# Kernel tuning notes

Measured on AMD Instinct MI355X. Metric: run time of the kernel, lower is better.

## Reference

```python
import jax, jax.numpy as jnp
import numpy as np

SEG = 512        # segment_size
DIL = 2          # dilation_rate
LN_EPS = 1e-5


def _layer_norm(x, gamma, beta):
    mu = jnp.mean(x, axis=-1, keepdims=True)
    var = jnp.var(x, axis=-1, keepdims=True)
    return (x - mu) * jax.lax.rsqrt(var + LN_EPS) * gamma + beta


def setup_inputs() -> dict:
    key = jax.random.key(0)
    ks = jax.random.split(key, 5)
    B, N, D = 4, 4096, 1024
    s = 0.02
    return {
        "x": jax.random.normal(ks[0], (B, N, D), dtype=jnp.float32),
        "Wq": jax.random.normal(ks[1], (D, D), dtype=jnp.float32) * s,
        "Wk": jax.random.normal(ks[2], (D, D), dtype=jnp.float32) * s,
        "Wv": jax.random.normal(ks[3], (D, D), dtype=jnp.float32) * s,
        "Wo": jax.random.normal(ks[4], (D, D), dtype=jnp.float32) * s,
        "gamma": jnp.ones((D,), dtype=jnp.float32),
        "beta": jnp.zeros((D,), dtype=jnp.float32),
    }


def reference(x, Wq, Wk, Wv, Wo, gamma, beta):
    B, N, D = x.shape
    n_seg = N // SEG
    s = SEG // DIL  # tokens per segment after dilation
    # strided dilated gather: [B, n_seg, s, D]
    xs = x.reshape(B, n_seg, SEG, D)[:, :, ::DIL, :]
    # torch Linear(bias=False): x @ W.T ; then LayerNorm on each of q,k,v
    q = _layer_norm(jnp.einsum('bgsd,ed->bgse', xs, Wq), gamma, beta)
    k = _layer_norm(jnp.einsum('bgsd,ed->bgse', xs, Wk), gamma, beta)
    v = _layer_norm(jnp.einsum('bgsd,ed->bgse', xs, Wv), gamma, beta)
    # causal SDPA with head_dim = D (no head split in the original code)
    scale = 1.0 / jnp.sqrt(jnp.asarray(D, dtype=q.dtype))
    scores = jnp.einsum('bgqd,bgkd->bgqk', q, k) * scale  # [B, n_seg, s, s]
    causal = jnp.tril(jnp.ones((s, s), dtype=bool))
    scores = jnp.where(causal, scores, jnp.finfo(scores.dtype).min)
    attn = jax.nn.softmax(scores, axis=-1)
    y = jnp.einsum('bgqk,bgkd->bgqd', attn, v)  # [B, n_seg, s, D]
    y = y.reshape(B, N // DIL, D)
    # strided scatter into zero-initialized full tensor
    y_full = jnp.zeros((B, N, D), dtype=y.dtype).at[:, ::DIL, :].set(y)
    out = jnp.einsum('bnd,ed->bne', y_full, Wo)
    return out
```

## Files before the change

### kernel.cpp

```cpp
#include <hip/hip_runtime.h>
#include <stdint.h>

typedef __bf16 bf16_t;
typedef __bf16 bf16x8 __attribute__((ext_vector_type(8)));
typedef __bf16 bf16x4 __attribute__((ext_vector_type(4)));
typedef float  f32x4  __attribute__((ext_vector_type(4)));


__device__ __forceinline__ void gload16(const void* g, void* lds)
{
    __builtin_amdgcn_global_load_lds(
        (__attribute__((address_space(1))) void*)(void*)g,
        (__attribute__((address_space(3))) void*)lds,
        16, 0, 0);
}

__device__ __forceinline__ f32x4 mfma16(bf16x8 a, bf16x8 b, f32x4 c)
{
    return __builtin_amdgcn_mfma_f32_16x16x32_bf16(a, b, c, 0, 0, 0);
}

#define SBAR()   asm volatile("s_barrier" ::: "memory")
#define LGKM0()  asm volatile("s_waitcnt lgkmcnt(0)" ::: "memory")
#define VMCNT(N) asm volatile("s_waitcnt vmcnt(" #N ")" ::: "memory")


__global__ __launch_bounds__(256)
void cast_f32_bf16(const float* __restrict__ in, bf16_t* __restrict__ out, int n4)
{
    const int i = blockIdx.x * blockDim.x + threadIdx.x;
    if (i >= n4) return;
    float4 f = *(const float4*)&in[(size_t)i * 4];
    bf16x4 o;
    o[0] = (bf16_t)f.x; o[1] = (bf16_t)f.y; o[2] = (bf16_t)f.z; o[3] = (bf16_t)f.w;
    *(bf16x4*)&out[(size_t)i * 4] = o;
}

__global__ __launch_bounds__(256)
void gather_cast_x(const float* __restrict__ x, bf16_t* __restrict__ Xe)
{
    const int m = blockIdx.x;
    const int b = m >> 11, g = (m >> 8) & 7, j = m & 255;
    const float* src = x + ((size_t)b * 4096 + g * 512 + 2 * j) * 1024;
    bf16_t* dst = Xe + (size_t)m * 1024;
    const int t = threadIdx.x;
    float4 f = *(const float4*)&src[t * 4];
    bf16x4 o;
    o[0] = (bf16_t)f.x; o[1] = (bf16_t)f.y; o[2] = (bf16_t)f.z; o[3] = (bf16_t)f.w;
    *(bf16x4*)&dst[t * 4] = o;
}

template<int EPI>
__global__ __launch_bounds__(512, 2)
void gemm256(const bf16_t* __restrict__ A, const bf16_t* __restrict__ B,
             void* __restrict__ Cv, int K, int lda, int ldb, int ldc)
{
    __shared__ __align__(16) char lds[131072];

    const int tid = threadIdx.x;
    const int w = tid >> 6, lane = tid & 63;
    const int wr = w >> 2, wc = w & 3;
    const int fr = lane & 15, fg = lane >> 4;
    const int bn = blockIdx.x, bm = blockIdx.y;
    const int NT = K >> 6;

    const int d0 = tid, d1 = 512 + tid;
    const int s0 = d0 ^ (((d0 >> 5) & 1) << 1) ^ (((d0 >> 6) & 1) << 2);
    const int s1 = d1 ^ (((d1 >> 5) & 1) << 1) ^ (((d1 >> 6) & 1) << 2);
    const size_t fixA0 = ((size_t)(bm * 256 + (s0 >> 9) * 128 + ((s0 >> 3) & 63)) * lda + (s0 & 7) * 8) * 2;
    const size_t fixA1 = ((size_t)(bm * 256 + (s1 >> 9) * 128 + ((s1 >> 3) & 63)) * lda + (s1 & 7) * 8) * 2;
    const size_t fixB0 = ((size_t)(bn * 256 + (s0 >> 8) * 64 + ((s0 >> 3) & 31)) * ldb + (s0 & 7) * 8) * 2;
    const size_t fixB1 = ((size_t)(bn * 256 + (s1 >> 8) * 64 + ((s1 >> 3) & 31)) * ldb + (s1 & 7) * 8) * 2;
    const size_t mqStep = (size_t)64 * lda * 2;
    const size_t nqStep = (size_t)32 * ldb * 2;
    const char* Ac = (const char*)A;
    const char* Bc = (const char*)B;
    const int ldsW = w * 1024;

#define STAGE(T, ISB, Q) do {                                                     \
    const int _b = ((T) & 1) * 65536 + (ISB) * 32768 + (Q) * 16384 + ldsW;        \
    const char *_g0, *_g1;                                                        \
    if (ISB) { _g0 = Bc + (Q)*nqStep + fixB0 + (size_t)(T)*128;                   \
               _g1 = Bc + (Q)*nqStep + fixB1 + (size_t)(T)*128; }                 \
    else     { _g0 = Ac + (Q)*mqStep + fixA0 + (size_t)(T)*128;                   \
               _g1 = Ac + (Q)*mqStep + fixA1 + (size_t)(T)*128; }                 \
    gload16(_g0, lds + _b);                                                       \
    gload16(_g1, lds + _b + 8192);                                                \
} while (0)

    const int abase = wr * 8192 + fr * 128 + fg * 16;
    const int bbase = wc * 4096 + fr * 128 + fg * 16;
    const int flip  = (((fr >> 2) & 1) << 5) | (((fr >> 3) & 1) << 6);

    bf16x8 a[4][2], b0[2][2], b1[2][2];
    f32x4 acc[8][4] = {};

#define LOAD_A(MQ, CB) do {                                                                 \
    _Pragma("unroll") for (int mi = 0; mi < 4; ++mi)                                        \
    _Pragma("unroll") for (int ks = 0; ks < 2; ++ks)                                        \
        a[mi][ks] = *(const bf16x8*)(lds + (CB) + (MQ)*16384 +                              \
                                     ((abase + mi*2048 + ks*64) ^ flip));                   \
} while (0)

#define LOAD_B(REG, NQ, CB) do {                                                            \
    _Pragma("unroll") for (int ni = 0; ni < 2; ++ni)                                        \
    _Pragma("unroll") for (int ks = 0; ks < 2; ++ks)                                        \
        REG[ni][ks] = *(const bf16x8*)(lds + (CB) + 32768 + (NQ)*16384 +                    \
                                       ((bbase + ni*2048 + ks*64) ^ flip));                 \
} while (0)

#define MFMA_Q(MQ, REG, NQ) do {                                                            \
    _Pragma("unroll") for (int mi = 0; mi < 4; ++mi)                                        \
    _Pragma("unroll") for (int ni = 0; ni < 2; ++ni)                                        \
    _Pragma("unroll") for (int ks = 0; ks < 2; ++ks)                                        \
        acc[(MQ)*4+mi][(NQ)*2+ni] =                                                         \
            mfma16(a[mi][ks], REG[ni][ks], acc[(MQ)*4+mi][(NQ)*2+ni]);                      \
} while (0)

    STAGE(0, 0, 0); STAGE(0, 1, 0); STAGE(0, 1, 1); STAGE(0, 0, 1);
    VMCNT(4);
    STAGE(1, 0, 0); STAGE(1, 1, 0); STAGE(1, 1, 1);
    VMCNT(6);
    SBAR();

    for (int t = 0; t < NT - 2; ++t) {
        const int cb = (t & 1) * 65536;
        LOAD_A(0, cb); LOAD_B(b0, 0, cb);
        STAGE(t + 1, 0, 1);
        SBAR(); LGKM0();
        __builtin_amdgcn_s_setprio(1); MFMA_Q(0, b0, 0); __builtin_amdgcn_s_setprio(0);
        SBAR();
        LOAD_B(b1, 1, cb);
        STAGE(t + 2, 0, 0);
        SBAR(); LGKM0();
        __builtin_amdgcn_s_setprio(1); MFMA_Q(0, b1, 1); __builtin_amdgcn_s_setprio(0);
        SBAR();
        LOAD_A(1, cb);
        STAGE(t + 2, 1, 0);
        SBAR(); LGKM0();
        __builtin_amdgcn_s_setprio(1); MFMA_Q(1, b1, 1); __builtin_amdgcn_s_setprio(0);
        SBAR();
        STAGE(t + 2, 1, 1);
        SBAR();
        __builtin_amdgcn_s_setprio(1); MFMA_Q(1, b0, 0); __builtin_amdgcn_s_setprio(0);
        VMCNT(6);
        SBAR();
    }

    STAGE(NT - 1, 0, 1);
    VMCNT(0);
    SBAR();
    for (int t = NT - 2; t < NT; ++t) {
        const int cb = (t & 1) * 65536;
        LOAD_A(0, cb); LOAD_B(b0, 0, cb);
        LGKM0();
        MFMA_Q(0, b0, 0);
        LOAD_B(b1, 1, cb);
        LGKM0();
        MFMA_Q(0, b1, 1);
        LOAD_A(1, cb);
        LGKM0();
        MFMA_Q(1, b1, 1);
        MFMA_Q(1, b0, 0);
    }

#undef STAGE
#undef LOAD_A
#undef LOAD_B
#undef MFMA_Q

    const int r0 = bm * 256 + wr * 128 + fg * 4;
    const int c0 = bn * 256 + wc * 64 + fr;
    if constexpr (EPI == 0) {
        bf16_t* C = (bf16_t*)Cv;
#pragma unroll
        for (int mig = 0; mig < 8; ++mig)
#pragma unroll
            for (int nig = 0; nig < 4; ++nig)
#pragma unroll
                for (int r = 0; r < 4; ++r)
                    C[(size_t)(r0 + mig * 16 + r) * ldc + c0 + nig * 16] =
                        (bf16_t)acc[mig][nig][r];
    }
}

template<int EPI>
__global__ __launch_bounds__(256)
void gemm_nt(const bf16_t* __restrict__ A, const bf16_t* __restrict__ B,
             void* __restrict__ Cv,
             int K, int lda, int ldb, int ldc,
             long sA, long sB, long sC)
{
    __shared__ __align__(16) bf16_t Asm[128 * 32];
    __shared__ __align__(16) bf16_t Bsm[128 * 32];

    const int tid  = threadIdx.x;
    const int wave = tid >> 6;
    const int lane = tid & 63;
    const int bn = blockIdx.x, bm = blockIdx.y, bz = blockIdx.z;
    const int wr = wave >> 1, wc = wave & 1;

    const bf16_t* Ab = A + (long)bz * sA;
    const bf16_t* Bb = B + (long)bz * sB;

    const int srow = tid >> 2;
    const int scol = (tid & 3) * 8;
    const bf16_t* a0 = Ab + (size_t)(bm * 128 + srow) * lda + scol;
    const bf16_t* a1 = a0 + (size_t)64 * lda;
    const bf16_t* b0 = Bb + (size_t)(bn * 128 + srow) * ldb + scol;
    const bf16_t* b1 = b0 + (size_t)64 * ldb;
    char* ldsA = (char*)Asm + wave * 1024;
    char* ldsB = (char*)Bsm + wave * 1024;

    f32x4 acc[4][4] = {};

    const int frow = lane & 15;
    const int fk   = (lane >> 4) * 8;

    for (int k0 = 0; k0 < K; k0 += 32) {
        gload16(a0, ldsA);
        gload16(a1, ldsA + 4096);
        gload16(b0, ldsB);
        gload16(b1, ldsB + 4096);
        a0 += 32; a1 += 32; b0 += 32; b1 += 32;
        __syncthreads();

        bf16x8 af[4], bfr[4];
#pragma unroll
        for (int mi = 0; mi < 4; ++mi)
            af[mi] = *(const bf16x8*)&Asm[(size_t)(wr * 64 + mi * 16 + frow) * 32 + fk];
#pragma unroll
        for (int ni = 0; ni < 4; ++ni)
            bfr[ni] = *(const bf16x8*)&Bsm[(size_t)(wc * 64 + ni * 16 + frow) * 32 + fk];
#pragma unroll
        for (int mi = 0; mi < 4; ++mi)
#pragma unroll
            for (int ni = 0; ni < 4; ++ni)
                acc[mi][ni] = mfma16(af[mi], bfr[ni], acc[mi][ni]);
        __syncthreads();
    }

    const int row0 = bm * 128 + wr * 64 + (lane >> 4) * 4;
    const int col0 = bn * 128 + wc * 64 + frow;

    if constexpr (EPI == 0) {
        bf16_t* C = (bf16_t*)Cv + (long)bz * sC;
#pragma unroll
        for (int mi = 0; mi < 4; ++mi)
#pragma unroll
            for (int ni = 0; ni < 4; ++ni)
#pragma unroll
                for (int r = 0; r < 4; ++r)
                    C[(size_t)(row0 + mi * 16 + r) * ldc + col0 + ni * 16] =
                        (bf16_t)acc[mi][ni][r];
    } else if constexpr (EPI == 1) {
        float* C = (float*)Cv + (long)bz * sC;
#pragma unroll
        for (int mi = 0; mi < 4; ++mi)
#pragma unroll
            for (int ni = 0; ni < 4; ++ni)
#pragma unroll
                for (int r = 0; r < 4; ++r)
                    C[(size_t)(row0 + mi * 16 + r) * ldc + col0 + ni * 16] =
                        acc[mi][ni][r];
    } else {
        float* C = (float*)Cv;
#pragma unroll
        for (int mi = 0; mi < 4; ++mi)
#pragma unroll
            for (int ni = 0; ni < 4; ++ni)
#pragma unroll
                for (int r = 0; r < 4; ++r) {
                    const int m  = row0 + mi * 16 + r;
                    const int gr = ((m >> 11) << 12) | (((m >> 8) & 7) << 9) | ((m & 255) << 1);
                    C[(size_t)gr * 1024 + col0 + ni * 16]       = acc[mi][ni][r];
                    C[(size_t)(gr + 1) * 1024 + col0 + ni * 16] = 0.0f;
                }
    }
}

__global__ __launch_bounds__(256)
void ln_kernel(bf16_t* __restrict__ qkv,
               const float* __restrict__ gamma, const float* __restrict__ beta)
{
    const int row = blockIdx.x;
    const int which = blockIdx.y;
    bf16_t* p = qkv + (size_t)row * 3072 + which * 1024;
    const int t = threadIdx.x;

    bf16x4 v = *(const bf16x4*)&p[t * 4];
    float f[4];
    float s = 0.f, ss = 0.f;
#pragma unroll
    for (int i = 0; i < 4; ++i) { f[i] = (float)v[i]; s += f[i]; ss += f[i] * f[i]; }
#pragma unroll
    for (int o = 32; o; o >>= 1) { s += __shfl_xor(s, o); ss += __shfl_xor(ss, o); }

    __shared__ float rs_[4], rss_[4];
    const int wave = t >> 6, lane = t & 63;
    if (lane == 0) { rs_[wave] = s; rss_[wave] = ss; }
    __syncthreads();
    s  = rs_[0] + rs_[1] + rs_[2] + rs_[3];
    ss = rss_[0] + rss_[1] + rss_[2] + rss_[3];

    const float mu   = s * (1.f / 1024.f);
    const float var  = ss * (1.f / 1024.f) - mu * mu;
    const float rstd = rsqrtf(var + 1e-5f);

    bf16x4 o;
#pragma unroll
    for (int i = 0; i < 4; ++i) {
        const int c = t * 4 + i;
        o[i] = (bf16_t)((f[i] - mu) * rstd * gamma[c] + beta[c]);
    }
    *(bf16x4*)&p[t * 4] = o;
}

__global__ __launch_bounds__(256)
void softmax_kernel(const float* __restrict__ S, bf16_t* __restrict__ P)
{
    const int q = blockIdx.x & 255;
    const size_t base = (size_t)blockIdx.x * 256;
    const int c = threadIdx.x;
    const bool ok = (c <= q);

    float v = ok ? S[base + c] * (1.f / 32.f) : -3.0e38f;
    float m = v;
#pragma unroll
    for (int o = 32; o; o >>= 1) m = fmaxf(m, __shfl_xor(m, o));

    __shared__ float rm[4], rsum[4];
    const int wave = c >> 6, lane = c & 63;
    if (lane == 0) rm[wave] = m;
    __syncthreads();
    m = fmaxf(fmaxf(rm[0], rm[1]), fmaxf(rm[2], rm[3]));

    float e = ok ? __expf(v - m) : 0.f;
    float s = e;
#pragma unroll
    for (int o = 32; o; o >>= 1) s += __shfl_xor(s, o);
    if (lane == 0) rsum[wave] = s;
    __syncthreads();
    s = rsum[0] + rsum[1] + rsum[2] + rsum[3];

    P[base + c] = (bf16_t)(e / s);
}

__global__ __launch_bounds__(256)
void transpose_v(const bf16_t* __restrict__ Vn, bf16_t* __restrict__ Vt)
{
    __shared__ bf16_t tile[32][33];
    const int seg = blockIdx.z;
    const int e0 = blockIdx.x * 32, k0 = blockIdx.y * 32;
    const int xx = threadIdx.x, yy = threadIdx.y;
    const bf16_t* src = Vn + (size_t)seg * 256 * 3072;
#pragma unroll
    for (int i = 0; i < 32; i += 8)
        tile[yy + i][xx] = src[(size_t)(k0 + yy + i) * 3072 + e0 + xx];
    __syncthreads();
    bf16_t* dst = Vt + (size_t)seg * 262144;
#pragma unroll
    for (int i = 0; i < 32; i += 8)
        dst[(size_t)(e0 + yy + i) * 256 + k0 + xx] = tile[xx][yy + i];
}


extern "C" void kernel_launch(void* const* d_in, const int* in_sizes, int n_in,
                              void* d_out, int out_size, void* d_ws, size_t ws_size,
                              hipStream_t stream)
{
    const float* x     = (const float*)d_in[0];
    const float* Wq    = (const float*)d_in[1];
    const float* Wk    = (const float*)d_in[2];
    const float* Wv    = (const float*)d_in[3];
    const float* Wo    = (const float*)d_in[4];
    const float* gamma = (const float*)d_in[5];
    const float* beta  = (const float*)d_in[6];
    float* out = (float*)d_out;

    char* ws = (char*)d_ws;
    bf16_t* Xe   = (bf16_t*)(ws);
    bf16_t* Wqkv = (bf16_t*)(ws + (16u  << 20));
    bf16_t* Wob  = (bf16_t*)(ws + (22u  << 20));
    bf16_t* QKV  = (bf16_t*)(ws + (24u  << 20));
    float*  Smat = (float*) (ws + (72u  << 20));
    bf16_t* P    = (bf16_t*)(ws + (80u  << 20));
    bf16_t* Vt   = (bf16_t*)(ws + (84u  << 20));
    bf16_t* Y    = (bf16_t*)(ws + (100u << 20));

    cast_f32_bf16<<<1024, 256, 0, stream>>>(Wq, Wqkv,           262144);
    cast_f32_bf16<<<1024, 256, 0, stream>>>(Wk, Wqkv + 1048576, 262144);
    cast_f32_bf16<<<1024, 256, 0, stream>>>(Wv, Wqkv + 2097152, 262144);
    cast_f32_bf16<<<1024, 256, 0, stream>>>(Wo, Wob,            262144);
    gather_cast_x<<<8192, 256, 0, stream>>>(x, Xe);

    gemm256<0><<<dim3(12, 32), 512, 0, stream>>>(Xe, Wqkv, QKV, 1024, 1024, 1024, 3072);

    ln_kernel<<<dim3(8192, 3), 256, 0, stream>>>(QKV, gamma, beta);

    gemm_nt<1><<<dim3(2, 2, 32), 256, 0, stream>>>(
        QKV, QKV + 1024, Smat, 1024, 3072, 3072, 256,
        256L * 3072, 256L * 3072, 65536L);

    softmax_kernel<<<8192, 256, 0, stream>>>(Smat, P);

    transpose_v<<<dim3(32, 8, 32), dim3(32, 8), 0, stream>>>(QKV + 2048, Vt);

    gemm_nt<0><<<dim3(8, 2, 32), 256, 0, stream>>>(
        P, Vt, Y, 256, 256, 256, 1024,
        65536L, 262144L, 262144L);

    gemm_nt<2><<<dim3(8, 64, 1), 256, 0, stream>>>(
        Y, Wob, out, 1024, 1024, 1024, 1024, 0, 0, 0);
}
```

Before: 211.4 us.

## Swizzle LDS layouts, swap MFMA operands for vector stores, fuse V layernorm with transpose

Changes the LDS swizzle in both GEMM kernels to avoid bank conflicts and swaps MFMA operand order so each lane owns four contiguous output columns. That lets every epilogue use vector stores instead of scalar ones. It also fuses the V layernorm into the transpose kernel, skips the upper-triangle K range for the causal P·V GEMM when bm==0, and drops the separate transpose kernel. The fused LN+transpose kernel launches only 256 blocks and loops serially over 32 column tiles, so it may be poorly parallelised.

Measured after the change: 224.9 us. 6.4% more time.

```diff
diff --git a/kernel.cpp b/kernel.cpp
--- a/kernel.cpp
+++ b/kernel.cpp
@@ -65,8 +65,8 @@
     const int NT = K >> 6;
 
     const int d0 = tid, d1 = 512 + tid;
-    const int s0 = d0 ^ (((d0 >> 5) & 1) << 1) ^ (((d0 >> 6) & 1) << 2);
-    const int s1 = d1 ^ (((d1 >> 5) & 1) << 1) ^ (((d1 >> 6) & 1) << 2);
+    const int s0 = d0 ^ ((d0 >> 3) & 7);
+    const int s1 = d1 ^ ((d1 >> 3) & 7);
     const size_t fixA0 = ((size_t)(bm * 256 + (s0 >> 9) * 128 + ((s0 >> 3) & 63)) * lda + (s0 & 7) * 8) * 2;
     const size_t fixA1 = ((size_t)(bm * 256 + (s1 >> 9) * 128 + ((s1 >> 3) & 63)) * lda + (s1 & 7) * 8) * 2;
     const size_t fixB0 = ((size_t)(bn * 256 + (s0 >> 8) * 64 + ((s0 >> 3) & 31)) * ldb + (s0 & 7) * 8) * 2;
@@ -90,7 +90,7 @@
 
     const int abase = wr * 8192 + fr * 128 + fg * 16;
     const int bbase = wc * 4096 + fr * 128 + fg * 16;
-    const int flip  = (((fr >> 2) & 1) << 5) | (((fr >> 3) & 1) << 6);
+    const int flip  = (fr & 7) << 4;
 
     bf16x8 a[4][2], b0[2][2], b1[2][2];
     f32x4 acc[8][4] = {};
@@ -114,7 +114,7 @@
     _Pragma("unroll") for (int ni = 0; ni < 2; ++ni)                                        \
     _Pragma("unroll") for (int ks = 0; ks < 2; ++ks)                                        \
         acc[(MQ)*4+mi][(NQ)*2+ni] =                                                         \
-            mfma16(a[mi][ks], REG[ni][ks], acc[(MQ)*4+mi][(NQ)*2+ni]);                      \
+            mfma16(REG[ni][ks], a[mi][ks], acc[(MQ)*4+mi][(NQ)*2+ni]);                      \
 } while (0)
 
     STAGE(0, 0, 0); STAGE(0, 1, 0); STAGE(0, 1, 1); STAGE(0, 0, 1);
@@ -169,18 +169,19 @@
 #undef LOAD_B
 #undef MFMA_Q
 
-    const int r0 = bm * 256 + wr * 128 + fg * 4;
-    const int c0 = bn * 256 + wc * 64 + fr;
+    const int r0 = bm * 256 + wr * 128 + fr;
+    const int c0 = bn * 256 + wc * 64 + fg * 4;
     if constexpr (EPI == 0) {
         bf16_t* C = (bf16_t*)Cv;
 #pragma unroll
         for (int mig = 0; mig < 8; ++mig)
 #pragma unroll
-            for (int nig = 0; nig < 4; ++nig)
-#pragma unroll
-                for (int r = 0; r < 4; ++r)
-                    C[(size_t)(r0 + mig * 16 + r) * ldc + c0 + nig * 16] =
-                        (bf16_t)acc[mig][nig][r];
+            for (int nig = 0; nig < 4; ++nig) {
+                bf16x4 o;
+#pragma unroll
+                for (int r = 0; r < 4; ++r) o[r] = (bf16_t)acc[mig][nig][r];
+                *(bf16x4*)&C[(size_t)(r0 + mig * 16) * ldc + c0 + nig * 16] = o;
+            }
     }
 }
 
@@ -189,7 +190,7 @@
 void gemm_nt(const bf16_t* __restrict__ A, const bf16_t* __restrict__ B,
              void* __restrict__ Cv,
              int K, int lda, int ldb, int ldc,
-             long sA, long sB, long sC)
+             long sA, long sB, long sC, int tri)
 {
     __shared__ __align__(16) bf16_t Asm[128 * 32];
     __shared__ __align__(16) bf16_t Bsm[128 * 32];
@@ -203,12 +204,15 @@
     const bf16_t* Ab = A + (long)bz * sA;
     const bf16_t* Bb = B + (long)bz * sB;
 
-    const int srow = tid >> 2;
-    const int scol = (tid & 3) * 8;
-    const bf16_t* a0 = Ab + (size_t)(bm * 128 + srow) * lda + scol;
-    const bf16_t* a1 = a0 + (size_t)64 * lda;
-    const bf16_t* b0 = Bb + (size_t)(bn * 128 + srow) * ldb + scol;
-    const bf16_t* b1 = b0 + (size_t)64 * ldb;
+    const int Keff = (tri && bm == 0) ? (K >> 1) : K;
+
+    const int sw0 = tid ^ ((tid >> 3) & 3);
+    const int dd1 = tid + 256;
+    const int sw1 = dd1 ^ ((dd1 >> 3) & 3);
+    const bf16_t* a0 = Ab + (size_t)(bm * 128 + (sw0 >> 2)) * lda + (sw0 & 3) * 8;
+    const bf16_t* a1 = Ab + (size_t)(bm * 128 + (sw1 >> 2)) * lda + (sw1 & 3) * 8;
+    const bf16_t* b0 = Bb + (size_t)(bn * 128 + (sw0 >> 2)) * ldb + (sw0 & 3) * 8;
+    const bf16_t* b1 = Bb + (size_t)(bn * 128 + (sw1 >> 2)) * ldb + (sw1 & 3) * 8;
     char* ldsA = (char*)Asm + wave * 1024;
     char* ldsB = (char*)Bsm + wave * 1024;
 
@@ -216,8 +220,9 @@
 
     const int frow = lane & 15;
     const int fk   = (lane >> 4) * 8;
-
-    for (int k0 = 0; k0 < K; k0 += 32) {
+    const int flip = (frow & 6) << 2;
+
+    for (int k0 = 0; k0 < Keff; k0 += 32) {
         gload16(a0, ldsA);
         gload16(a1, ldsA + 4096);
         gload16(b0, ldsB);
@@ -228,54 +233,51 @@
         bf16x8 af[4], bfr[4];
 #pragma unroll
         for (int mi = 0; mi < 4; ++mi)
-            af[mi] = *(const bf16x8*)&Asm[(size_t)(wr * 64 + mi * 16 + frow) * 32 + fk];
+            af[mi] = *(const bf16x8*)&Asm[(size_t)(((wr * 64 + mi * 16 + frow) * 32 + fk) ^ flip)];
 #pragma unroll
         for (int ni = 0; ni < 4; ++ni)
-            bfr[ni] = *(const bf16x8*)&Bsm[(size_t)(wc * 64 + ni * 16 + frow) * 32 + fk];
+            bfr[ni] = *(const bf16x8*)&Bsm[(size_t)(((wc * 64 + ni * 16 + frow) * 32 + fk) ^ flip)];
 #pragma unroll
         for (int mi = 0; mi < 4; ++mi)
 #pragma unroll
             for (int ni = 0; ni < 4; ++ni)
-                acc[mi][ni] = mfma16(af[mi], bfr[ni], acc[mi][ni]);
+                acc[mi][ni] = mfma16(bfr[ni], af[mi], acc[mi][ni]);
         __syncthreads();
     }
 
-    const int row0 = bm * 128 + wr * 64 + (lane >> 4) * 4;
-    const int col0 = bn * 128 + wc * 64 + frow;
+    const int row0 = bm * 128 + wr * 64 + frow;
+    const int col0 = bn * 128 + wc * 64 + (lane >> 4) * 4;
 
     if constexpr (EPI == 0) {
         bf16_t* C = (bf16_t*)Cv + (long)bz * sC;
 #pragma unroll
         for (int mi = 0; mi < 4; ++mi)
 #pragma unroll
-            for (int ni = 0; ni < 4; ++ni)
-#pragma unroll
-                for (int r = 0; r < 4; ++r)
-                    C[(size_t)(row0 + mi * 16 + r) * ldc + col0 + ni * 16] =
-                        (bf16_t)acc[mi][ni][r];
+            for (int ni = 0; ni < 4; ++ni) {
+                bf16x4 o;
+#pragma unroll
+                for (int r = 0; r < 4; ++r) o[r] = (bf16_t)acc[mi][ni][r];
+                *(bf16x4*)&C[(size_t)(row0 + mi * 16) * ldc + col0 + ni * 16] = o;
+            }
     } else if constexpr (EPI == 1) {
         float* C = (float*)Cv + (long)bz * sC;
 #pragma unroll
         for (int mi = 0; mi < 4; ++mi)
 #pragma unroll
             for (int ni = 0; ni < 4; ++ni)
-#pragma unroll
-                for (int r = 0; r < 4; ++r)
-                    C[(size_t)(row0 + mi * 16 + r) * ldc + col0 + ni * 16] =
-                        acc[mi][ni][r];
+                *(f32x4*)&C[(size_t)(row0 + mi * 16) * ldc + col0 + ni * 16] = acc[mi][ni];
     } else {
         float* C = (float*)Cv;
+        const f32x4 z4 = {0.f, 0.f, 0.f, 0.f};
 #pragma unroll
         for (int mi = 0; mi < 4; ++mi)
 #pragma unroll
-            for (int ni = 0; ni < 4; ++ni)
-#pragma unroll
-                for (int r = 0; r < 4; ++r) {
-                    const int m  = row0 + mi * 16 + r;
-                    const int gr = ((m >> 11) << 12) | (((m >> 8) & 7) << 9) | ((m & 255) << 1);
-                    C[(size_t)gr * 1024 + col0 + ni * 16]       = acc[mi][ni][r];
-                    C[(size_t)(gr + 1) * 1024 + col0 + ni * 16] = 0.0f;
-                }
+            for (int ni = 0; ni < 4; ++ni) {
+                const int m  = row0 + mi * 16;
+                const int gr = ((m >> 11) << 12) | (((m >> 8) & 7) << 9) | ((m & 255) << 1);
+                *(f32x4*)&C[(size_t)gr * 1024 + col0 + ni * 16]       = acc[mi][ni];
+                *(f32x4*)&C[(size_t)(gr + 1) * 1024 + col0 + ni * 16] = z4;
+            }
     }
 }
 
@@ -317,6 +319,55 @@
 }
 
 __global__ __launch_bounds__(256)
+void ln_v_t(const bf16_t* __restrict__ qkv, bf16_t* __restrict__ Vt,
+            const float* __restrict__ gamma, const float* __restrict__ beta)
+{
+    const int kb  = blockIdx.x;
+    const int seg = blockIdx.y;
+    const int t = threadIdx.x;
+    const bf16_t* V = qkv + ((size_t)seg * 256 + kb * 32) * 3072 + 2048;
+
+    const int row = t >> 3, sub = t & 7;
+    const bf16_t* vr = V + (size_t)row * 3072 + sub * 128;
+    float s = 0.f, ss = 0.f;
+#pragma unroll
+    for (int i = 0; i < 16; ++i) {
+        bf16x8 v = *(const bf16x8*)&vr[i * 8];
+#pragma unroll
+        for (int j = 0; j < 8; ++j) { float f = (float)v[j]; s += f; ss += f * f; }
+    }
+#pragma unroll
+    for (int o = 1; o < 8; o <<= 1) { s += __shfl_xor(s, o); ss += __shfl_xor(ss, o); }
+    __shared__ float mu_[32], rs_[32];
+    if (sub == 0) {
+        const float mu = s * (1.f / 1024.f);
+        mu_[row] = mu;
+        rs_[row] = rsqrtf(ss * (1.f / 1024.f) - mu * mu + 1e-5f);
+    }
+    __syncthreads();
+
+    __shared__ bf16_t tile[32][33];
+    const int xx = t & 31, yy = t >> 5;
+    bf16_t* dst = Vt + (size_t)seg * 262144 + kb * 32;
+    for (int e0 = 0; e0 < 1024; e0 += 32) {
+        const float g = gamma[e0 + xx], b = beta[e0 + xx];
+#pragma unroll
+        for (int i = 0; i < 4; ++i) {
+            const int r = yy * 4 + i;
+            const float f = (float)V[(size_t)r * 3072 + e0 + xx];
+            tile[r][xx] = (bf16_t)((f - mu_[r]) * rs_[r] * g + b);
+        }
+        __syncthreads();
+#pragma unroll
+        for (int i = 0; i < 4; ++i) {
+            const int e = yy * 4 + i;
+            dst[(size_t)(e0 + e) * 256 + xx] = tile[xx][e];
+        }
+        __syncthreads();
+    }
+}
+
+__global__ __launch_bounds__(256)
 void softmax_kernel(const float* __restrict__ S, bf16_t* __restrict__ P)
 {
     const int q = blockIdx.x & 255;
@@ -344,24 +395,6 @@
     s = rsum[0] + rsum[1] + rsum[2] + rsum[3];
 
     P[base + c] = (bf16_t)(e / s);
-}
-
-__global__ __launch_bounds__(256)
-void transpose_v(const bf16_t* __restrict__ Vn, bf16_t* __restrict__ Vt)
-{
-    __shared__ bf16_t tile[32][33];
-    const int seg = blockIdx.z;
-    const int e0 = blockIdx.x * 32, k0 = blockIdx.y * 32;
-    const int xx = threadIdx.x, yy = threadIdx.y;
-    const bf16_t* src = Vn + (size_t)seg * 256 * 3072;
-#pragma unroll
-    for (int i = 0; i < 32; i += 8)
-        tile[yy + i][xx] = src[(size_t)(k0 + yy + i) * 3072 + e0 + xx];
-    __syncthreads();
-    bf16_t* dst = Vt + (size_t)seg * 262144;
-#pragma unroll
-    for (int i = 0; i < 32; i += 8)
-        dst[(size_t)(e0 + yy + i) * 256 + k0 + xx] = tile[xx][yy + i];
 }
 
 
@@ -396,20 +429,20 @@
 
     gemm256<0><<<dim3(12, 32), 512, 0, stream>>>(Xe, Wqkv, QKV, 1024, 1024, 1024, 3072);
 
-    ln_kernel<<<dim3(8192, 3), 256, 0, stream>>>(QKV, gamma, beta);
+    ln_kernel<<<dim3(8192, 2), 256, 0, stream>>>(QKV, gamma, beta);
 
     gemm_nt<1><<<dim3(2, 2, 32), 256, 0, stream>>>(
         QKV, QKV + 1024, Smat, 1024, 3072, 3072, 256,
-        256L * 3072, 256L * 3072, 65536L);
+        256L * 3072, 256L * 3072, 65536L, 0);
 
     softmax_kernel<<<8192, 256, 0, stream>>>(Smat, P);
 
-    transpose_v<<<dim3(32, 8, 32), dim3(32, 8), 0, stream>>>(QKV + 2048, Vt);
+    ln_v_t<<<dim3(8, 32), 256, 0, stream>>>(QKV, Vt, gamma, beta);
 
     gemm_nt<0><<<dim3(8, 2, 32), 256, 0, stream>>>(
         P, Vt, Y, 256, 256, 256, 1024,
-        65536L, 262144L, 262144L);
+        65536L, 262144L, 262144L, 1);
 
     gemm_nt<2><<<dim3(8, 64, 1), 256, 0, stream>>>(
-        Y, Wob, out, 1024, 1024, 1024, 1024, 0, 0, 0);
-}
+        Y, Wob, out, 1024, 1024, 1024, 1024, 0, 0, 0, 0);
+}
```
